# Performance work log

Measured on AMD Instinct MI355X. Metric: run time of the kernel, lower is better.

The kernel has to match this reference:

```python
import jax, jax.numpy as jnp
import numpy as np

jax.config.update("jax_enable_x64", True)

NUM_PARTS = 4
N_CAD = 8192
N_CAM = 8192


def setup_inputs() -> dict:
    key = jax.random.key(0)
    ks = jax.random.split(key, 7)
    cad_pts = jax.random.normal(ks[0], (NUM_PARTS, N_CAD, 3), jnp.float32)
    camera_pts = jax.random.normal(ks[1], (NUM_PARTS, N_CAM, 3), jnp.float32)
    part_weight = jax.random.uniform(ks[2], (NUM_PARTS,), jnp.float32)
    rot_quats = jax.random.normal(ks[3], (NUM_PARTS, 4), jnp.float32)  # [w,x,y,z] per part
    tras = 0.1 * jax.random.normal(ks[4], (NUM_PARTS, 3, 1), jnp.float32)
    rt_k = jnp.eye(4, dtype=jnp.float32)[None] + 0.01 * jax.random.normal(ks[5], (NUM_PARTS, 4, 4), jnp.float32)
    joint_axes = jax.random.normal(ks[6], (NUM_PARTS - 1, 2, 4), jnp.float32)
    return {"camera_pts": camera_pts, "cad_pts": cad_pts, "part_weight": part_weight,
            "rot_quats": rot_quats, "tras": tras, "rt_k": rt_k, "joint_axes": joint_axes}


def _quat_to_rot(q):
    # q = [w, x, y, z] -> a,b,c,d as in the torch code
    q = q / jnp.linalg.norm(q)
    a, b, c, d = q[0], q[1], q[2], q[3]
    return jnp.stack([
        1 - 2 * c * c - 2 * d * d, 2 * b * c - 2 * a * d, 2 * a * c + 2 * b * d,
        2 * b * c + 2 * a * d, 1 - 2 * b * b - 2 * d * d, 2 * c * d - 2 * a * b,
        2 * b * d - 2 * a * c, 2 * a * b + 2 * c * d, 1 - 2 * b * b - 2 * c * c,
    ]).reshape(3, 3)


def _chamfer(x, y):
    # symmetric Chamfer (mean of k=1 NN distances both ways), in float64 like torch code
    x = x.astype(jnp.float64)
    y = y.astype(jnp.float64)
    x2 = jnp.sum(x * x, axis=1)  # [N]
    y2 = jnp.sum(y * y, axis=1)  # [M]
    d2 = x2[:, None] + y2[None, :] - 2.0 * (x @ y.T)  # [N,M]
    d = jnp.sqrt(jnp.maximum(d2, 0.0))
    return jnp.min(d, axis=1).mean() + jnp.min(d, axis=0).mean()


def _forward(camera_pts, cad_pts, part_weight, rot_quats, tras, rt_k, joint_axes):
    P = cad_pts.shape[0]
    f32 = jnp.float32
    # homogeneous coords [P,N,4] / [P,M,4]
    scad = jnp.concatenate([cad_pts, jnp.ones(cad_pts.shape[:2] + (1,), f32)], axis=-1)
    scam = jnp.concatenate([camera_pts, jnp.ones(camera_pts.shape[:2] + (1,), f32)], axis=-1)

    rots = jax.vmap(_quat_to_rot)(rot_quats)                       # [P,3,3]
    top = jnp.concatenate([rots, tras], axis=2)                    # [P,3,4]
    bottom = jnp.broadcast_to(jnp.array([[[0.0, 0.0, 0.0, 1.0]]], f32), (P, 1, 4))
    transforms = jnp.concatenate([top, bottom], axis=1)            # [P,4,4]

    cad_base = jnp.einsum('pij,pnj->pni', transforms, scad)        # [P,N,4]
    e_geo = jax.vmap(_chamfer)(cad_base, scam)                     # [P] float64
    eners = 5.0 * e_geo                                            # [P]

    # torch.tensor(eners) detaches -> stop_gradient
    et = jax.lax.stop_gradient(eners)
    et = (et - jnp.min(et)) / (jnp.max(et) - jnp.min(et) + 1e-8)
    sm = jax.nn.softmax(et, axis=0)                                # [P] float64

    errors_p = part_weight.astype(jnp.float64) * sm * eners        # [P]
    all_obj = jnp.sum(sm * eners)

    # ---- E_kin ----
    x_t = jnp.einsum('pij,pnj->pni', transforms, scad)             # [P,N,4]
    distances = jnp.linalg.norm(x_t - scam, axis=-1).mean(axis=-1).mean()
    Tj_q = rt_k[0] @ transforms[0] @ joint_axes[0, 0]              # [4] (fixed index 0, as in source)
    Tj1_q = jnp.einsum('pij,pjk,pk->pi', rt_k[1:], transforms[1:], joint_axes[:, 1])  # [P-1,4]
    diff = (Tj_q[None, :] - Tj1_q)[:, :3]                          # [P-1,3]
    nrm = jnp.linalg.norm(diff) / P
    e_kin = jnp.log(0.1 * nrm + 1.0) + distances

    e_kin_total = jnp.max(errors_p) * e_kin
    all_obj = all_obj + e_kin_total
    errors = jnp.concatenate([errors_p, e_kin_total[None]])        # [P+1]
    return all_obj, errors, jax.lax.stop_gradient(transforms)


def reference(camera_pts, cad_pts, part_weight, rot_quats, tras, rt_k, joint_axes):
    return _forward(camera_pts, cad_pts, part_weight, rot_quats, tras, rt_k, joint_axes)
```

## Files before the change

kernel.cpp:

```cpp
#include <hip/hip_runtime.h>
#include <cstdint>
#include <math.h>

#define NPARTS 4
#define NPTS   8192
#define YSPLIT 16

#define WS_SUMS_OFF 256
#define WS_PART_OFF 384

typedef float f32x2 __attribute__((ext_vector_type(2)));
typedef float f32x4 __attribute__((ext_vector_type(4)));

__device__ __forceinline__ f32x2 pk_fma(f32x2 a, f32x2 b, f32x2 c) {
    f32x2 d;
    asm("v_pk_fma_f32 %0, %1, %2, %3" : "=v"(d) : "v"(a), "v"(b), "v"(c));
    return d;
}
__device__ __forceinline__ float min3f(float a, float b, float c) {
    float d;
    asm("v_min3_f32 %0, %1, %2, %3" : "=v"(d) : "v"(a), "v"(b), "v"(c));
    return d;
}

__global__ __launch_bounds__(256) void k_setup(const float* __restrict__ rot_quats,
                                               const float* __restrict__ tras,
                                               float* __restrict__ ws,
                                               float* __restrict__ out) {
    if (threadIdx.x >= 16 && threadIdx.x < 25) {
        double* s = (double*)((char*)ws + WS_SUMS_OFF);
        s[threadIdx.x - 16] = 0.0;
    }
    if (threadIdx.x < NPARTS) {
        int p = threadIdx.x;
        double q0 = rot_quats[p*4+0], q1 = rot_quats[p*4+1];
        double q2 = rot_quats[p*4+2], q3 = rot_quats[p*4+3];
        double inv = 1.0 / sqrt(q0*q0 + q1*q1 + q2*q2 + q3*q3);
        double a = q0*inv, b = q1*inv, c = q2*inv, d = q3*inv;
        float T[16];
        T[0]  = (float)(1.0 - 2.0*c*c - 2.0*d*d);
        T[1]  = (float)(2.0*b*c - 2.0*a*d);
        T[2]  = (float)(2.0*a*c + 2.0*b*d);
        T[3]  = tras[p*3+0];
        T[4]  = (float)(2.0*b*c + 2.0*a*d);
        T[5]  = (float)(1.0 - 2.0*b*b - 2.0*d*d);
        T[6]  = (float)(2.0*c*d - 2.0*a*b);
        T[7]  = tras[p*3+1];
        T[8]  = (float)(2.0*b*d - 2.0*a*c);
        T[9]  = (float)(2.0*a*b + 2.0*c*d);
        T[10] = (float)(1.0 - 2.0*b*b - 2.0*c*c);
        T[11] = tras[p*3+2];
        T[12] = 0.f; T[13] = 0.f; T[14] = 0.f; T[15] = 1.f;
        #pragma unroll
        for (int i = 0; i < 16; ++i) {
            ws[p*16 + i] = T[i];
            out[6 + p*16 + i] = T[i];
        }
    }
}

__global__ __launch_bounds__(256, 4) void k_chamfer(const float* __restrict__ cam,
                                                    const float* __restrict__ cad,
                                                    float* __restrict__ ws) {
    constexpr int TPB = 256, REG_X = 8;
    constexpr int XTILE = TPB * REG_X;
    constexpr int XTILES = NPTS / XTILE;
    constexpr int YLEN = NPTS / YSPLIT;
    __shared__ f32x4 ybuf4[4][YLEN / 4];

    float* partial = (float*)((char*)ws + WS_PART_OFF);

    int b   = blockIdx.x;
    int ysi = b & (YSPLIT - 1);
    int xt  = (b / YSPLIT) & (XTILES - 1);
    int dir = (b / (YSPLIT * XTILES)) & 1;
    int p   = b / (YSPLIT * XTILES * 2);

    float T[12];
    #pragma unroll
    for (int i = 0; i < 12; ++i) T[i] = ws[p*16 + i];

    const float* xsrc = (dir == 0) ? cad + (size_t)p*NPTS*3 : cam + (size_t)p*NPTS*3;
    const float* ysrc = (dir == 0) ? cam + (size_t)p*NPTS*3 : cad + (size_t)p*NPTS*3;

    for (int j = threadIdx.x; j < YLEN; j += TPB) {
        int yi = ysi * YLEN + j;
        float v0 = ysrc[yi*3+0], v1 = ysrc[yi*3+1], v2 = ysrc[yi*3+2];
        if (dir == 1) {
            float w0 = T[0]*v0 + T[1]*v1 + T[2]*v2 + T[3];
            float w1 = T[4]*v0 + T[5]*v1 + T[6]*v2 + T[7];
            float w2 = T[8]*v0 + T[9]*v1 + T[10]*v2 + T[11];
            v0 = w0; v1 = w1; v2 = w2;
        }
        ((float*)ybuf4[0])[j] = -2.f * v0;
        ((float*)ybuf4[1])[j] = -2.f * v1;
        ((float*)ybuf4[2])[j] = -2.f * v2;
        ((float*)ybuf4[3])[j] = v0*v0 + v1*v1 + v2*v2;
    }

    f32x2 x0pk[REG_X], x1pk[REG_X], x2pk[REG_X];
    #pragma unroll
    for (int r = 0; r < REG_X; ++r) {
        int xi = xt*XTILE + r*TPB + threadIdx.x;
        float v0 = xsrc[xi*3+0], v1 = xsrc[xi*3+1], v2 = xsrc[xi*3+2];
        if (dir == 0) {
            float w0 = T[0]*v0 + T[1]*v1 + T[2]*v2 + T[3];
            float w1 = T[4]*v0 + T[5]*v1 + T[6]*v2 + T[7];
            float w2 = T[8]*v0 + T[9]*v1 + T[10]*v2 + T[11];
            v0 = w0; v1 = w1; v2 = w2;
        }
        x0pk[r] = (f32x2){v0, v0};
        x1pk[r] = (f32x2){v1, v1};
        x2pk[r] = (f32x2){v2, v2};
    }

    float mn[REG_X];
    #pragma unroll
    for (int r = 0; r < REG_X; ++r) mn[r] = INFINITY;

    __syncthreads();

    for (int g = 0; g < YLEN / 4; ++g) {
        f32x4 c0 = ybuf4[0][g];
        f32x4 c1 = ybuf4[1][g];
        f32x4 c2 = ybuf4[2][g];
        f32x4 qq = ybuf4[3][g];
        f32x2 c0lo = __builtin_shufflevector(c0, c0, 0, 1), c0hi = __builtin_shufflevector(c0, c0, 2, 3);
        f32x2 c1lo = __builtin_shufflevector(c1, c1, 0, 1), c1hi = __builtin_shufflevector(c1, c1, 2, 3);
        f32x2 c2lo = __builtin_shufflevector(c2, c2, 0, 1), c2hi = __builtin_shufflevector(c2, c2, 2, 3);
        f32x2 qqlo = __builtin_shufflevector(qq, qq, 0, 1), qqhi = __builtin_shufflevector(qq, qq, 2, 3);
        #pragma unroll
        for (int r = 0; r < REG_X; ++r) {
            f32x2 t = pk_fma(x0pk[r], c0lo, qqlo);
            t = pk_fma(x1pk[r], c1lo, t);
            t = pk_fma(x2pk[r], c2lo, t);
            mn[r] = min3f(mn[r], t.x, t.y);
            f32x2 u = pk_fma(x0pk[r], c0hi, qqhi);
            u = pk_fma(x1pk[r], c1hi, u);
            u = pk_fma(x2pk[r], c2hi, u);
            mn[r] = min3f(mn[r], u.x, u.y);
        }
    }

    float* slab = partial + (size_t)((dir*NPARTS + p)*YSPLIT + ysi) * NPTS;
    #pragma unroll
    for (int r = 0; r < REG_X; ++r) {
        int xi = xt*XTILE + r*TPB + threadIdx.x;
        float v0 = x0pk[r].x, v1 = x1pk[r].x, v2 = x2pk[r].x;
        float d2 = fmaxf(v0*v0 + v1*v1 + v2*v2 + mn[r], 0.f);
        slab[xi] = d2;
    }
}

__global__ __launch_bounds__(256) void k_reduce(const float* __restrict__ cam,
                                                const float* __restrict__ cad,
                                                float* __restrict__ ws) {
    __shared__ double red[256];
    double local = 0.0;
    int b = blockIdx.x;
    if (b < 64) {
        const float* partial = (const float*)((const char*)ws + WS_PART_OFF);
        int dir   = b >> 5;
        int p     = (b >> 3) & 3;
        int chunk = b & 7;
        const float* base = partial + (size_t)(dir*NPARTS + p) * YSPLIT * NPTS;
        #pragma unroll
        for (int k = 0; k < 4; ++k) {
            int x = chunk*1024 + k*256 + threadIdx.x;
            float mnv = INFINITY;
            #pragma unroll
            for (int ysi = 0; ysi < YSPLIT; ++ysi)
                mnv = fminf(mnv, base[(size_t)ysi*NPTS + x]);
            local += sqrt((double)mnv);
        }
        red[threadIdx.x] = local;
        __syncthreads();
        for (int s = 128; s > 0; s >>= 1) {
            if (threadIdx.x < s) red[threadIdx.x] += red[threadIdx.x + s];
            __syncthreads();
        }
        if (threadIdx.x == 0) {
            double* sums = (double*)((char*)ws + WS_SUMS_OFF);
            atomicAdd(&sums[p*2 + dir], red[0]);
        }
    } else {
        int gid = (b - 64) * 256 + threadIdx.x;
        int p = gid >> 13;
        float T[12];
        #pragma unroll
        for (int i = 0; i < 12; ++i) T[i] = ws[p*16 + i];
        float v0 = cad[gid*3+0], v1 = cad[gid*3+1], v2 = cad[gid*3+2];
        float w0 = T[0]*v0 + T[1]*v1 + T[2]*v2 + T[3];
        float w1 = T[4]*v0 + T[5]*v1 + T[6]*v2 + T[7];
        float w2 = T[8]*v0 + T[9]*v1 + T[10]*v2 + T[11];
        float d0 = w0 - cam[gid*3+0];
        float d1 = w1 - cam[gid*3+1];
        float d2 = w2 - cam[gid*3+2];
        local = sqrt((double)(d0*d0 + d1*d1 + d2*d2));
        red[threadIdx.x] = local;
        __syncthreads();
        for (int s = 128; s > 0; s >>= 1) {
            if (threadIdx.x < s) red[threadIdx.x] += red[threadIdx.x + s];
            __syncthreads();
        }
        if (threadIdx.x == 0) {
            double* dist_sum = (double*)((char*)ws + WS_SUMS_OFF) + 8;
            atomicAdd(dist_sum, red[0]);
        }
    }
}

__global__ void k_final(const float* __restrict__ pw,
                        const float* __restrict__ rtk,
                        const float* __restrict__ ja,
                        const float* __restrict__ ws,
                        float* __restrict__ out) {
    const double* sums = (const double*)((const char*)ws + WS_SUMS_OFF);
    double eners[NPARTS];
    for (int p = 0; p < NPARTS; ++p)
        eners[p] = 5.0 * ((sums[p*2+0] + sums[p*2+1]) / (double)NPTS);

    double mn = eners[0], mx = eners[0];
    for (int p = 1; p < NPARTS; ++p) { mn = fmin(mn, eners[p]); mx = fmax(mx, eners[p]); }
    double et[NPARTS], etmax = -1e300;
    for (int p = 0; p < NPARTS; ++p) { et[p] = (eners[p] - mn) / (mx - mn + 1e-8); etmax = fmax(etmax, et[p]); }
    double ex[NPARTS], se = 0.0;
    for (int p = 0; p < NPARTS; ++p) { ex[p] = exp(et[p] - etmax); se += ex[p]; }

    double ep[NPARTS], all_obj = 0.0, epmax = -1e300;
    for (int p = 0; p < NPARTS; ++p) {
        double sm = ex[p] / se;
        ep[p] = (double)pw[p] * sm * eners[p];
        all_obj += sm * eners[p];
        epmax = fmax(epmax, ep[p]);
    }

    double distances = sums[8] / (double)(NPARTS * NPTS);

    double v[4], Tj[4], ss = 0.0;
    for (int i = 0; i < 4; ++i) {
        v[i] = 0.0;
        for (int k = 0; k < 4; ++k) v[i] += (double)ws[0*16 + i*4 + k] * (double)ja[0*8 + 0*4 + k];
    }
    for (int i = 0; i < 4; ++i) {
        Tj[i] = 0.0;
        for (int k = 0; k < 4; ++k) Tj[i] += (double)rtk[0*16 + i*4 + k] * v[k];
    }
    for (int q = 1; q < NPARTS; ++q) {
        double vv[4], u[4];
        for (int i = 0; i < 4; ++i) {
            vv[i] = 0.0;
            for (int k = 0; k < 4; ++k) vv[i] += (double)ws[q*16 + i*4 + k] * (double)ja[(q-1)*8 + 4 + k];
        }
        for (int i = 0; i < 4; ++i) {
            u[i] = 0.0;
            for (int k = 0; k < 4; ++k) u[i] += (double)rtk[q*16 + i*4 + k] * vv[k];
        }
        for (int i = 0; i < 3; ++i) { double dd = Tj[i] - u[i]; ss += dd * dd; }
    }
    double nrm = sqrt(ss) / (double)NPARTS;
    double e_kin = log(0.1 * nrm + 1.0) + distances;
    double ekt = epmax * e_kin;
    all_obj += ekt;

    out[0] = (float)all_obj;
    for (int p = 0; p < NPARTS; ++p) out[1 + p] = (float)ep[p];
    out[5] = (float)ekt;
}

extern "C" void kernel_launch(void* const* d_in, const int* in_sizes, int n_in,
                              void* d_out, int out_size, void* d_ws, size_t ws_size,
                              hipStream_t stream) {
    const float* cam  = (const float*)d_in[0];
    const float* cad  = (const float*)d_in[1];
    const float* pw   = (const float*)d_in[2];
    const float* rq   = (const float*)d_in[3];
    const float* tras = (const float*)d_in[4];
    const float* rtk  = (const float*)d_in[5];
    const float* ja   = (const float*)d_in[6];
    float* out = (float*)d_out;
    float* ws  = (float*)d_ws;

    hipLaunchKernelGGL(k_setup,   dim3(1),   dim3(256), 0, stream, rq, tras, ws, out);
    hipLaunchKernelGGL(k_chamfer, dim3(512), dim3(256), 0, stream, cam, cad, ws);
    hipLaunchKernelGGL(k_reduce,  dim3(192), dim3(256), 0, stream, cam, cad, ws);
    hipLaunchKernelGGL(k_final,   dim3(1),   dim3(1),   0, stream, pw, rtk, ja, ws, out);
}
```

Measured before the change: 56.64 us.

## Compute both Chamfer directions from one distance tile with row and column minima

The old kernel evaluated the cad-to-cam and cam-to-cad nearest-neighbour searches separately, computing every pairwise distance twice. The new chamfer kernel evaluates each distance tile once and keeps both per-row and per-column minima, reducing column minima through shared memory and writing partial mins for a later reduction. A new pre-pass transforms the cad points and lays out the cam points as structure-of-arrays planes, and it also folds in the E_kin distance term. The cost is extra shared-memory reduction work and syncs per 64-point chunk, extra launches and a memset, plus larger workspace traffic. The setup kernel also drops from double to single precision for the quaternion-to-rotation math.

```diff
diff --git a/kernel.cpp b/kernel.cpp
--- a/kernel.cpp
+++ b/kernel.cpp
@@ -4,10 +4,22 @@
 
 #define NPARTS 4
 #define NPTS   8192
+
+#define TPB    256
+#define RX     8
+#define RY     8
+#define XB     256
+#define YCHUNK 64
+#define YSEG   512
 #define YSPLIT 16
-
-#define WS_SUMS_OFF 256
-#define WS_PART_OFF 384
+#define XT     32
+
+#define WS_T_OFF      0
+#define WS_SUMS_OFF   256
+#define WS_CADT_OFF   512
+#define WS_CAMP_OFF   (WS_CADT_OFF + 524288)
+#define WS_ROWMIN_OFF (WS_CAMP_OFF + 524288)
+#define WS_COLMIN_OFF (WS_ROWMIN_OFF + 2097152)
 
 typedef float f32x2 __attribute__((ext_vector_type(2)));
 typedef float f32x4 __attribute__((ext_vector_type(4)));
@@ -27,28 +39,24 @@
                                                const float* __restrict__ tras,
                                                float* __restrict__ ws,
                                                float* __restrict__ out) {
-    if (threadIdx.x >= 16 && threadIdx.x < 25) {
-        double* s = (double*)((char*)ws + WS_SUMS_OFF);
-        s[threadIdx.x - 16] = 0.0;
-    }
     if (threadIdx.x < NPARTS) {
         int p = threadIdx.x;
-        double q0 = rot_quats[p*4+0], q1 = rot_quats[p*4+1];
-        double q2 = rot_quats[p*4+2], q3 = rot_quats[p*4+3];
-        double inv = 1.0 / sqrt(q0*q0 + q1*q1 + q2*q2 + q3*q3);
-        double a = q0*inv, b = q1*inv, c = q2*inv, d = q3*inv;
+        float q0 = rot_quats[p*4+0], q1 = rot_quats[p*4+1];
+        float q2 = rot_quats[p*4+2], q3 = rot_quats[p*4+3];
+        float inv = 1.0f / sqrtf(q0*q0 + q1*q1 + q2*q2 + q3*q3);
+        float a = q0*inv, b = q1*inv, c = q2*inv, d = q3*inv;
         float T[16];
-        T[0]  = (float)(1.0 - 2.0*c*c - 2.0*d*d);
-        T[1]  = (float)(2.0*b*c - 2.0*a*d);
-        T[2]  = (float)(2.0*a*c + 2.0*b*d);
+        T[0]  = 1.f - 2.f*c*c - 2.f*d*d;
+        T[1]  = 2.f*b*c - 2.f*a*d;
+        T[2]  = 2.f*a*c + 2.f*b*d;
         T[3]  = tras[p*3+0];
-        T[4]  = (float)(2.0*b*c + 2.0*a*d);
-        T[5]  = (float)(1.0 - 2.0*b*b - 2.0*d*d);
-        T[6]  = (float)(2.0*c*d - 2.0*a*b);
+        T[4]  = 2.f*b*c + 2.f*a*d;
+        T[5]  = 1.f - 2.f*b*b - 2.f*d*d;
+        T[6]  = 2.f*c*d - 2.f*a*b;
         T[7]  = tras[p*3+1];
-        T[8]  = (float)(2.0*b*d - 2.0*a*c);
-        T[9]  = (float)(2.0*a*b + 2.0*c*d);
-        T[10] = (float)(1.0 - 2.0*b*b - 2.0*c*c);
+        T[8]  = 2.f*b*d - 2.f*a*c;
+        T[9]  = 2.f*a*b + 2.f*c*d;
+        T[10] = 1.f - 2.f*b*b - 2.f*c*c;
         T[11] = tras[p*3+2];
         T[12] = 0.f; T[13] = 0.f; T[14] = 0.f; T[15] = 1.f;
         #pragma unroll
@@ -59,154 +67,180 @@
     }
 }
 
-__global__ __launch_bounds__(256, 4) void k_chamfer(const float* __restrict__ cam,
-                                                    const float* __restrict__ cad,
-                                                    float* __restrict__ ws) {
-    constexpr int TPB = 256, REG_X = 8;
-    constexpr int XTILE = TPB * REG_X;
-    constexpr int XTILES = NPTS / XTILE;
-    constexpr int YLEN = NPTS / YSPLIT;
-    __shared__ f32x4 ybuf4[4][YLEN / 4];
-
-    float* partial = (float*)((char*)ws + WS_PART_OFF);
-
-    int b   = blockIdx.x;
-    int ysi = b & (YSPLIT - 1);
-    int xt  = (b / YSPLIT) & (XTILES - 1);
-    int dir = (b / (YSPLIT * XTILES)) & 1;
-    int p   = b / (YSPLIT * XTILES * 2);
-
-    float T[12];
+__global__ __launch_bounds__(256) void k_pre(const float* __restrict__ cam,
+                                             const float* __restrict__ cad,
+                                             float* __restrict__ ws) {
+    int gid = blockIdx.x * 256 + threadIdx.x;
+    int p = gid >> 13;
+    int i = gid & (NPTS - 1);
+    const float* T = ws + p*16;
+    float v0 = cad[(size_t)gid*3+0], v1 = cad[(size_t)gid*3+1], v2 = cad[(size_t)gid*3+2];
+    float w0 = fmaf(T[0],v0, fmaf(T[1],v1, fmaf(T[2],v2, T[3])));
+    float w1 = fmaf(T[4],v0, fmaf(T[5],v1, fmaf(T[6],v2, T[7])));
+    float w2 = fmaf(T[8],v0, fmaf(T[9],v1, fmaf(T[10],v2, T[11])));
+    f32x4* cadT = (f32x4*)((char*)ws + WS_CADT_OFF);
+    cadT[gid] = (f32x4){w0, w1, w2, w0*w0 + w1*w1 + w2*w2};
+
+    float c0 = cam[(size_t)gid*3+0], c1 = cam[(size_t)gid*3+1], c2 = cam[(size_t)gid*3+2];
+    float* camP = (float*)((char*)ws + WS_CAMP_OFF) + (size_t)p*4*NPTS;
+    camP[0*NPTS + i] = -2.f*c0;
+    camP[1*NPTS + i] = -2.f*c1;
+    camP[2*NPTS + i] = -2.f*c2;
+    camP[3*NPTS + i] = c0*c0 + c1*c1 + c2*c2;
+
+    float d0 = w0 - c0, d1 = w1 - c1, d2 = w2 - c2;
+    double local = sqrt((double)(d0*d0 + d1*d1 + d2*d2));
+    __shared__ double red[256];
+    red[threadIdx.x] = local;
+    __syncthreads();
+    for (int s = 128; s > 0; s >>= 1) {
+        if (threadIdx.x < s) red[threadIdx.x] += red[threadIdx.x + s];
+        __syncthreads();
+    }
+    if (threadIdx.x == 0) {
+        double* dist_sum = (double*)((char*)ws + WS_SUMS_OFF) + 8;
+        atomicAdd(dist_sum, red[0]);
+    }
+}
+
+__global__ __launch_bounds__(TPB, 4) void k_chamfer(float* __restrict__ ws) {
+    const int tid = threadIdx.x;
+    const int tx = tid & 31, ty = tid >> 5;
+    const int b = blockIdx.x;
+    const int ysi = b & (YSPLIT - 1);
+    const int xt  = (b >> 4) & (XT - 1);
+    const int p   = b >> 9;
+
+    const f32x4* cadT = (const f32x4*)((char*)ws + WS_CADT_OFF) + (size_t)p*NPTS;
+    const float* camP = (const float*)((char*)ws + WS_CAMP_OFF) + (size_t)p*4*NPTS;
+    float* rowming = (float*)((char*)ws + WS_ROWMIN_OFF) + ((size_t)(p*YSPLIT + ysi))*NPTS + xt*XB;
+    float* colming = (float*)((char*)ws + WS_COLMIN_OFF) + ((size_t)(p*XT + xt))*NPTS;
+
+    __shared__ f32x4 yp4[4][YCHUNK/4];
+    __shared__ float scr[XB*9];
+
+    f32x2 X0[RX], X1[RX], X2[RX];
+    float XS[RX];
     #pragma unroll
-    for (int i = 0; i < 12; ++i) T[i] = ws[p*16 + i];
-
-    const float* xsrc = (dir == 0) ? cad + (size_t)p*NPTS*3 : cam + (size_t)p*NPTS*3;
-    const float* ysrc = (dir == 0) ? cam + (size_t)p*NPTS*3 : cad + (size_t)p*NPTS*3;
-
-    for (int j = threadIdx.x; j < YLEN; j += TPB) {
-        int yi = ysi * YLEN + j;
-        float v0 = ysrc[yi*3+0], v1 = ysrc[yi*3+1], v2 = ysrc[yi*3+2];
-        if (dir == 1) {
-            float w0 = T[0]*v0 + T[1]*v1 + T[2]*v2 + T[3];
-            float w1 = T[4]*v0 + T[5]*v1 + T[6]*v2 + T[7];
-            float w2 = T[8]*v0 + T[9]*v1 + T[10]*v2 + T[11];
-            v0 = w0; v1 = w1; v2 = w2;
-        }
-        ((float*)ybuf4[0])[j] = -2.f * v0;
-        ((float*)ybuf4[1])[j] = -2.f * v1;
-        ((float*)ybuf4[2])[j] = -2.f * v2;
-        ((float*)ybuf4[3])[j] = v0*v0 + v1*v1 + v2*v2;
-    }
-
-    f32x2 x0pk[REG_X], x1pk[REG_X], x2pk[REG_X];
+    for (int r = 0; r < RX; ++r) {
+        f32x4 v = cadT[xt*XB + r*32 + tx];
+        X0[r] = (f32x2){v.x, v.x};
+        X1[r] = (f32x2){v.y, v.y};
+        X2[r] = (f32x2){v.z, v.z};
+        XS[r] = v.w;
+    }
+    float rm[RX];
     #pragma unroll
-    for (int r = 0; r < REG_X; ++r) {
-        int xi = xt*XTILE + r*TPB + threadIdx.x;
-        float v0 = xsrc[xi*3+0], v1 = xsrc[xi*3+1], v2 = xsrc[xi*3+2];
-        if (dir == 0) {
-            float w0 = T[0]*v0 + T[1]*v1 + T[2]*v2 + T[3];
-            float w1 = T[4]*v0 + T[5]*v1 + T[6]*v2 + T[7];
-            float w2 = T[8]*v0 + T[9]*v1 + T[10]*v2 + T[11];
-            v0 = w0; v1 = w1; v2 = w2;
-        }
-        x0pk[r] = (f32x2){v0, v0};
-        x1pk[r] = (f32x2){v1, v1};
-        x2pk[r] = (f32x2){v2, v2};
-    }
-
-    float mn[REG_X];
+    for (int r = 0; r < RX; ++r) rm[r] = INFINITY;
+
+    for (int chunk = 0; chunk < YSEG/YCHUNK; ++chunk) {
+        const int ybase = ysi*YSEG + chunk*YCHUNK;
+        if (tid < 64) {
+            int plane = tid >> 4, idx = tid & 15;
+            yp4[plane][idx] = *(const f32x4*)(camP + (size_t)plane*NPTS + ybase + idx*4);
+        }
+        __syncthreads();
+
+        float cmf[RY];
+        #pragma unroll
+        for (int k = 0; k < RY; ++k) cmf[k] = INFINITY;
+
+        #pragma unroll
+        for (int g = 0; g < 2; ++g) {
+            int ys4 = ty*2 + g;
+            f32x4 c0 = yp4[0][ys4];
+            f32x4 c1 = yp4[1][ys4];
+            f32x4 c2 = yp4[2][ys4];
+            f32x4 qq = yp4[3][ys4];
+            f32x2 c0lo = __builtin_shufflevector(c0, c0, 0,1), c0hi = __builtin_shufflevector(c0, c0, 2,3);
+            f32x2 c1lo = __builtin_shufflevector(c1, c1, 0,1), c1hi = __builtin_shufflevector(c1, c1, 2,3);
+            f32x2 c2lo = __builtin_shufflevector(c2, c2, 0,1), c2hi = __builtin_shufflevector(c2, c2, 2,3);
+            f32x2 qqlo = __builtin_shufflevector(qq, qq, 0,1), qqhi = __builtin_shufflevector(qq, qq, 2,3);
+            #pragma unroll
+            for (int r = 0; r < RX; r += 2) {
+                f32x2 ta = pk_fma(X0[r],   c0lo, qqlo); ta = pk_fma(X1[r],   c1lo, ta); ta = pk_fma(X2[r],   c2lo, ta);
+                f32x2 tb = pk_fma(X0[r+1], c0lo, qqlo); tb = pk_fma(X1[r+1], c1lo, tb); tb = pk_fma(X2[r+1], c2lo, tb);
+                rm[r]   = min3f(rm[r],   ta.x, ta.y);
+                rm[r+1] = min3f(rm[r+1], tb.x, tb.y);
+                cmf[g*4+0] = min3f(cmf[g*4+0], ta.x + XS[r], tb.x + XS[r+1]);
+                cmf[g*4+1] = min3f(cmf[g*4+1], ta.y + XS[r], tb.y + XS[r+1]);
+                f32x2 ua = pk_fma(X0[r],   c0hi, qqhi); ua = pk_fma(X1[r],   c1hi, ua); ua = pk_fma(X2[r],   c2hi, ua);
+                f32x2 ub = pk_fma(X0[r+1], c0hi, qqhi); ub = pk_fma(X1[r+1], c1hi, ub); ub = pk_fma(X2[r+1], c2hi, ub);
+                rm[r]   = min3f(rm[r],   ua.x, ua.y);
+                rm[r+1] = min3f(rm[r+1], ub.x, ub.y);
+                cmf[g*4+2] = min3f(cmf[g*4+2], ua.x + XS[r], ub.x + XS[r+1]);
+                cmf[g*4+3] = min3f(cmf[g*4+3], ua.y + XS[r], ub.y + XS[r+1]);
+            }
+        }
+
+        #pragma unroll
+        for (int k = 0; k < RY; ++k) scr[(ty*8+k)*33 + tx] = cmf[k];
+        __syncthreads();
+        if (tid < YCHUNK) {
+            float m = INFINITY;
+            #pragma unroll
+            for (int j = 0; j < 32; ++j) m = fminf(m, scr[tid*33 + j]);
+            colming[ybase + tid] = m;
+        }
+        __syncthreads();
+    }
+
     #pragma unroll
-    for (int r = 0; r < REG_X; ++r) mn[r] = INFINITY;
-
+    for (int r = 0; r < RX; ++r) scr[(r*32+tx)*9 + ty] = rm[r];
     __syncthreads();
-
-    for (int g = 0; g < YLEN / 4; ++g) {
-        f32x4 c0 = ybuf4[0][g];
-        f32x4 c1 = ybuf4[1][g];
-        f32x4 c2 = ybuf4[2][g];
-        f32x4 qq = ybuf4[3][g];
-        f32x2 c0lo = __builtin_shufflevector(c0, c0, 0, 1), c0hi = __builtin_shufflevector(c0, c0, 2, 3);
-        f32x2 c1lo = __builtin_shufflevector(c1, c1, 0, 1), c1hi = __builtin_shufflevector(c1, c1, 2, 3);
-        f32x2 c2lo = __builtin_shufflevector(c2, c2, 0, 1), c2hi = __builtin_shufflevector(c2, c2, 2, 3);
-        f32x2 qqlo = __builtin_shufflevector(qq, qq, 0, 1), qqhi = __builtin_shufflevector(qq, qq, 2, 3);
-        #pragma unroll
-        for (int r = 0; r < REG_X; ++r) {
-            f32x2 t = pk_fma(x0pk[r], c0lo, qqlo);
-            t = pk_fma(x1pk[r], c1lo, t);
-            t = pk_fma(x2pk[r], c2lo, t);
-            mn[r] = min3f(mn[r], t.x, t.y);
-            f32x2 u = pk_fma(x0pk[r], c0hi, qqhi);
-            u = pk_fma(x1pk[r], c1hi, u);
-            u = pk_fma(x2pk[r], c2hi, u);
-            mn[r] = min3f(mn[r], u.x, u.y);
-        }
-    }
-
-    float* slab = partial + (size_t)((dir*NPARTS + p)*YSPLIT + ysi) * NPTS;
-    #pragma unroll
-    for (int r = 0; r < REG_X; ++r) {
-        int xi = xt*XTILE + r*TPB + threadIdx.x;
-        float v0 = x0pk[r].x, v1 = x1pk[r].x, v2 = x2pk[r].x;
-        float d2 = fmaxf(v0*v0 + v1*v1 + v2*v2 + mn[r], 0.f);
-        slab[xi] = d2;
-    }
-}
-
-__global__ __launch_bounds__(256) void k_reduce(const float* __restrict__ cam,
-                                                const float* __restrict__ cad,
-                                                float* __restrict__ ws) {
+    {
+        float m = INFINITY;
+        #pragma unroll
+        for (int t = 0; t < 8; ++t) m = fminf(m, scr[tid*9 + t]);
+        rowming[tid] = m;
+    }
+}
+
+__global__ __launch_bounds__(256) void k_reduce(float* __restrict__ ws) {
     __shared__ double red[256];
     double local = 0.0;
-    int b = blockIdx.x;
-    if (b < 64) {
-        const float* partial = (const float*)((const char*)ws + WS_PART_OFF);
-        int dir   = b >> 5;
-        int p     = (b >> 3) & 3;
-        int chunk = b & 7;
-        const float* base = partial + (size_t)(dir*NPARTS + p) * YSPLIT * NPTS;
-        #pragma unroll
+    const int b = blockIdx.x;
+    const int tid = threadIdx.x;
+    if (b < 32) {
+        int p = b >> 3, seg = b & 7;
+        const float* rowmin = (const float*)((const char*)ws + WS_ROWMIN_OFF) + (size_t)p*YSPLIT*NPTS;
+        const f32x4* cadT = (const f32x4*)((const char*)ws + WS_CADT_OFF) + (size_t)p*NPTS;
         for (int k = 0; k < 4; ++k) {
-            int x = chunk*1024 + k*256 + threadIdx.x;
-            float mnv = INFINITY;
+            int row = seg*1024 + k*256 + tid;
+            float m = INFINITY;
             #pragma unroll
             for (int ysi = 0; ysi < YSPLIT; ++ysi)
-                mnv = fminf(mnv, base[(size_t)ysi*NPTS + x]);
-            local += sqrt((double)mnv);
-        }
-        red[threadIdx.x] = local;
+                m = fminf(m, rowmin[(size_t)ysi*NPTS + row]);
+            float d2 = fmaxf(m + cadT[row].w, 0.f);
+            local += sqrt((double)d2);
+        }
+        red[tid] = local;
         __syncthreads();
         for (int s = 128; s > 0; s >>= 1) {
-            if (threadIdx.x < s) red[threadIdx.x] += red[threadIdx.x + s];
+            if (tid < s) red[tid] += red[tid + s];
             __syncthreads();
         }
-        if (threadIdx.x == 0) {
-            double* sums = (double*)((char*)ws + WS_SUMS_OFF);
-            atomicAdd(&sums[p*2 + dir], red[0]);
-        }
+        if (tid == 0) atomicAdd((double*)((char*)ws + WS_SUMS_OFF) + p*2 + 0, red[0]);
     } else {
-        int gid = (b - 64) * 256 + threadIdx.x;
-        int p = gid >> 13;
-        float T[12];
-        #pragma unroll
-        for (int i = 0; i < 12; ++i) T[i] = ws[p*16 + i];
-        float v0 = cad[gid*3+0], v1 = cad[gid*3+1], v2 = cad[gid*3+2];
-        float w0 = T[0]*v0 + T[1]*v1 + T[2]*v2 + T[3];
-        float w1 = T[4]*v0 + T[5]*v1 + T[6]*v2 + T[7];
-        float w2 = T[8]*v0 + T[9]*v1 + T[10]*v2 + T[11];
-        float d0 = w0 - cam[gid*3+0];
-        float d1 = w1 - cam[gid*3+1];
-        float d2 = w2 - cam[gid*3+2];
-        local = sqrt((double)(d0*d0 + d1*d1 + d2*d2));
-        red[threadIdx.x] = local;
+        int q = b - 32;
+        int p = q >> 3, seg = q & 7;
+        const float* colmin = (const float*)((const char*)ws + WS_COLMIN_OFF) + (size_t)p*XT*NPTS;
+        for (int k = 0; k < 4; ++k) {
+            int y = seg*1024 + k*256 + tid;
+            float m = INFINITY;
+            #pragma unroll
+            for (int xt = 0; xt < XT; ++xt)
+                m = fminf(m, colmin[(size_t)xt*NPTS + y]);
+            float d2 = fmaxf(m, 0.f);
+            local += sqrt((double)d2);
+        }
+        red[tid] = local;
         __syncthreads();
         for (int s = 128; s > 0; s >>= 1) {
-            if (threadIdx.x < s) red[threadIdx.x] += red[threadIdx.x + s];
+            if (tid < s) red[tid] += red[tid + s];
             __syncthreads();
         }
-        if (threadIdx.x == 0) {
-            double* dist_sum = (double*)((char*)ws + WS_SUMS_OFF) + 8;
-            atomicAdd(dist_sum, red[0]);
-        }
+        if (tid == 0) atomicAdd((double*)((char*)ws + WS_SUMS_OFF) + p*2 + 1, red[0]);
     }
 }
 
@@ -281,8 +315,10 @@
     float* out = (float*)d_out;
     float* ws  = (float*)d_ws;
 
-    hipLaunchKernelGGL(k_setup,   dim3(1),   dim3(256), 0, stream, rq, tras, ws, out);
-    hipLaunchKernelGGL(k_chamfer, dim3(512), dim3(256), 0, stream, cam, cad, ws);
-    hipLaunchKernelGGL(k_reduce,  dim3(192), dim3(256), 0, stream, cam, cad, ws);
-    hipLaunchKernelGGL(k_final,   dim3(1),   dim3(1),   0, stream, pw, rtk, ja, ws, out);
-}
+    hipMemsetAsync((char*)ws + WS_SUMS_OFF, 0, 80, stream);
+    hipLaunchKernelGGL(k_setup,   dim3(1),    dim3(256), 0, stream, rq, tras, ws, out);
+    hipLaunchKernelGGL(k_pre,     dim3(128),  dim3(256), 0, stream, cam, cad, ws);
+    hipLaunchKernelGGL(k_chamfer, dim3(2048), dim3(256), 0, stream, ws);
+    hipLaunchKernelGGL(k_reduce,  dim3(64),   dim3(256), 0, stream, ws);
+    hipLaunchKernelGGL(k_final,   dim3(1),    dim3(1),   0, stream, pw, rtk, ja, ws, out);
+}
```

After: 56.80 us. Within noise of the previous version (+0.3%).
